# Performance work log

Measured on AMD Instinct MI355X. Metric: run time of the kernel, lower is better.

## Reference

```python
import jax, jax.numpy as jnp
import numpy as np

N = 10000      # num nodes
E = 320000     # num edges
IN = 256       # in_dim
MP = 256       # mp_width
FL = 512       # fl_width
OUT = 64       # out_dim


def setup_inputs() -> dict:
    key = jax.random.key(0)
    ks = jax.random.split(key, 20)
    inp = {}
    inp["x"] = jax.random.normal(ks[0], (N, IN), dtype=jnp.float32)
    inp["edge_index"] = jax.random.randint(ks[1], (2, E), 0, N, dtype=jnp.int64)
    # iMP (frozen) linear layers: weight ~ N(0, 1) per nn.init.normal_(std=1.0)
    inp["mp_w0"] = jax.random.normal(ks[2], (IN, MP), dtype=jnp.float32)
    inp["mp_b0"] = jax.random.uniform(ks[3], (MP,), minval=-1.0, maxval=1.0) / np.sqrt(IN)
    inp["mp_w1"] = jax.random.normal(ks[4], (MP, MP), dtype=jnp.float32)
    inp["mp_b1"] = jax.random.uniform(ks[5], (MP,), minval=-1.0, maxval=1.0) / np.sqrt(MP)
    inp["mp_w2"] = jax.random.normal(ks[6], (MP, MP), dtype=jnp.float32)
    inp["mp_b2"] = jax.random.uniform(ks[7], (MP,), minval=-1.0, maxval=1.0) / np.sqrt(MP)
    # FC layers (torch default Linear init scale ~ 1/sqrt(fan_in))
    inp["fc_w0"] = jax.random.normal(ks[8], (MP, FL), dtype=jnp.float32) / np.sqrt(MP)
    inp["fc_b0"] = jnp.zeros((FL,), dtype=jnp.float32)
    inp["fc_w1"] = jax.random.normal(ks[9], (FL, FL), dtype=jnp.float32) / np.sqrt(FL)
    inp["fc_b1"] = jnp.zeros((FL,), dtype=jnp.float32)
    # injection projections
    inp["inj_w0"] = jax.random.normal(ks[10], (MP, FL), dtype=jnp.float32) / np.sqrt(MP)
    inp["inj_b0"] = jnp.zeros((FL,), dtype=jnp.float32)
    inp["inj_w1"] = jax.random.normal(ks[11], (MP, FL), dtype=jnp.float32) / np.sqrt(MP)
    inp["inj_b1"] = jnp.zeros((FL,), dtype=jnp.float32)
    inp["alpha"] = jnp.array(1.0, dtype=jnp.float32)
    inp["out_w"] = jax.random.normal(ks[12], (FL, OUT), dtype=jnp.float32) / np.sqrt(FL)
    inp["out_b"] = jnp.zeros((OUT,), dtype=jnp.float32)
    return inp


def _imp(x, w, b, row, col, deg_inv):
    # h = relu(W x); h /= deg; Ah = scatter_add over row of h[col]
    h = jax.nn.relu(x @ w + b) * deg_inv[:, None]      # [N, out]
    return jnp.zeros_like(h).at[row].add(h[col])       # gather + scatter-add


def reference(x, edge_index, mp_w0, mp_b0, mp_w1, mp_b1, mp_w2, mp_b2,
              fc_w0, fc_b0, fc_w1, fc_b1, inj_w0, inj_b0, inj_w1, inj_b1,
              alpha, out_w, out_b):
    row, col = edge_index[0], edge_index[1]
    deg = jax.ops.segment_sum(jnp.ones((E,), x.dtype), col, num_segments=N)
    # nodes with deg==0 never appear in col so clamping does not change output
    deg_inv = 1.0 / jnp.maximum(deg, 1.0)

    h = _imp(x, mp_w0, mp_b0, row, col, deg_inv)
    h = _imp(h, mp_w1, mp_b1, row, col, deg_inv)
    h = _imp(h, mp_w2, mp_b2, row, col, deg_inv)

    x_inject = h
    h = alpha * (jax.nn.relu(h) @ fc_w0 + fc_b0) + (x_inject @ inj_w0 + inj_b0)
    h = alpha * (jax.nn.relu(h) @ fc_w1 + fc_b1) + (x_inject @ inj_w1 + inj_b1)
    return h @ out_w + out_b
```

## Files before the change

### kernel.cpp

```cpp
#include <hip/hip_runtime.h>

#define N_NODES 10000
#define N_EDGES 320000
#define MPAD 10048
#define NBIN 10048
#define CHUNK 4096
#define NCH 79

typedef unsigned short u16;
typedef short bf16x8 __attribute__((ext_vector_type(8)));
typedef float f32x4 __attribute__((ext_vector_type(4)));

__device__ __forceinline__ u16 f2b(float f) {
  unsigned u = __builtin_bit_cast(unsigned, f);
  unsigned r = u + 0x7fffu + ((u >> 16) & 1u);
  return (u16)(r >> 16);
}
__device__ __forceinline__ unsigned pack2(float a, float b) {
  return (unsigned)f2b(a) | ((unsigned)f2b(b) << 16);
}
__device__ __forceinline__ float blo(unsigned u) { return __builtin_bit_cast(float, u << 16); }
__device__ __forceinline__ float bhi(unsigned u) { return __builtin_bit_cast(float, u & 0xffff0000u); }

__global__ void prep(
    const float* __restrict__ x,
    const float* __restrict__ w0, const float* __restrict__ w1, const float* __restrict__ w2,
    const float* __restrict__ fcw0, const float* __restrict__ injw0,
    const float* __restrict__ fcw1, const float* __restrict__ injw1,
    const float* __restrict__ outw,
    const float* __restrict__ fcb0, const float* __restrict__ injb0,
    const float* __restrict__ fcb1, const float* __restrict__ injb1,
    const float* __restrict__ alpha_p,
    u16* __restrict__ xb, u16* __restrict__ w0t, u16* __restrict__ w1t, u16* __restrict__ w2t,
    u16* __restrict__ wc1t, u16* __restrict__ wc2t, u16* __restrict__ owt,
    float* __restrict__ bias1, float* __restrict__ bias2)
{
  long i = (long)blockIdx.x * 256 + threadIdx.x;
  const float alpha = alpha_p[0];
  if (i < 640000L) {
    float4 v = ((const float4*)x)[i];
    uint2 o;
    o.x = pack2(v.x, v.y);
    o.y = pack2(v.z, v.w);
    *(uint2*)(xb + 4 * i) = o;
    return;
  }
  i -= 640000L;
  if (i < 65536) { w0t[i] = f2b(w0[(i & 255) * 256 + (i >> 8)]); return; }
  i -= 65536;
  if (i < 65536) { w1t[i] = f2b(w1[(i & 255) * 256 + (i >> 8)]); return; }
  i -= 65536;
  if (i < 65536) { w2t[i] = f2b(w2[(i & 255) * 256 + (i >> 8)]); return; }
  i -= 65536;
  if (i < 262144) {
    int n = (int)(i >> 9), k = (int)(i & 511);
    float v = (k < 256) ? alpha * fcw0[k * 512 + n] : injw0[(k - 256) * 512 + n];
    wc1t[i] = f2b(v); return;
  }
  i -= 262144;
  if (i < 393216) {
    int n = (int)(i / 768), k = (int)(i % 768);
    float v = (k < 512) ? alpha * fcw1[k * 512 + n] : injw1[(k - 512) * 512 + n];
    wc2t[i] = f2b(v); return;
  }
  i -= 393216;
  if (i < 32768) {
    int n = (int)(i >> 9), k = (int)(i & 511);
    owt[i] = f2b(outw[k * 64 + n]); return;
  }
  i -= 32768;
  if (i < 512) { bias1[i] = alpha * fcb0[i] + injb0[i]; return; }
  i -= 512;
  if (i < 512) { bias2[i] = alpha * fcb1[i] + injb1[i]; return; }
}

__global__ __launch_bounds__(256) void edge_hist(const int* __restrict__ ei,
                                                 int* __restrict__ histR,
                                                 int* __restrict__ histC) {
  __shared__ int hr[NBIN], hc[NBIN];
  const int ch = blockIdx.x, t = threadIdx.x;
  for (int i = t; i < NBIN; i += 256) { hr[i] = 0; hc[i] = 0; }
  __syncthreads();
  const int e0 = ch * CHUNK;
#pragma unroll
  for (int j = 0; j < CHUNK; j += 256) {
    int e = e0 + j + t;
    if (e < N_EDGES) {
      atomicAdd(&hr[ei[e]], 1);
      atomicAdd(&hc[ei[N_EDGES + e]], 1);
    }
  }
  __syncthreads();
  for (int i = t; i < NBIN; i += 256) {
    histR[(size_t)ch * NBIN + i] = hr[i];
    histC[(size_t)ch * NBIN + i] = hc[i];
  }
}

__global__ __launch_bounds__(256) void col_scan(const int* __restrict__ histR,
                                                const int* __restrict__ histC,
                                                int* __restrict__ chunkoff,
                                                int* __restrict__ cntR,
                                                float* __restrict__ deg_inv) {
  int r = blockIdx.x * 256 + threadIdx.x;
  if (r >= NBIN) return;
  int run = 0, dg = 0;
  for (int ch = 0; ch < NCH; ++ch) {
    chunkoff[(size_t)ch * NBIN + r] = run;
    run += histR[(size_t)ch * NBIN + r];
    dg  += histC[(size_t)ch * NBIN + r];
  }
  cntR[r] = run;
  deg_inv[r] = 1.0f / (float)(dg > 1 ? dg : 1);
}

__global__ __launch_bounds__(1024) void row_scan(const int* __restrict__ cntR,
                                                 int* __restrict__ row_ptr) {
  const int t = threadIdx.x;
  const int i0 = t * 10;
  int v[10];
  int s = 0;
#pragma unroll
  for (int i = 0; i < 10; ++i) {
    int id = i0 + i;
    v[i] = (id < NBIN) ? cntR[id] : 0;
    s += v[i];
  }
  int lane = t & 63, wid = t >> 6;
  int incl = s;
#pragma unroll
  for (int off = 1; off < 64; off <<= 1) {
    int y = __shfl_up(incl, off, 64);
    if (lane >= off) incl += y;
  }
  __shared__ int wsum[16], wexc[16];
  if (lane == 63) wsum[wid] = incl;
  __syncthreads();
  if (t == 0) {
    int run = 0;
#pragma unroll
    for (int i = 0; i < 16; ++i) { wexc[i] = run; run += wsum[i]; }
  }
  __syncthreads();
  int run = wexc[wid] + incl - s;
#pragma unroll
  for (int i = 0; i < 10; ++i) {
    int id = i0 + i;
    if (id <= N_NODES) row_ptr[id] = run;
    run += v[i];
  }
}

__global__ __launch_bounds__(256) void place_edges(const int* __restrict__ ei,
                                                   const int* __restrict__ chunkoff,
                                                   const int* __restrict__ row_ptr,
                                                   int* __restrict__ csr) {
  __shared__ int cur[NBIN];
  const int ch = blockIdx.x, t = threadIdx.x;
  const int* co = chunkoff + (size_t)ch * NBIN;
  for (int i = t; i < NBIN; i += 256) cur[i] = co[i];
  __syncthreads();
  const int e0 = ch * CHUNK;
#pragma unroll
  for (int j = 0; j < CHUNK; j += 256) {
    int e = e0 + j + t;
    if (e < N_EDGES) {
      int r = ei[e];
      int c = ei[N_EDGES + e];
      int rank = atomicAdd(&cur[r], 1);
      csr[row_ptr[r] + rank] = c;
    }
  }
}

template<int K, bool RELU, bool SCALE, bool F32OUT>
__global__ __launch_bounds__(256) void gemm64(
    const u16* __restrict__ A, int lda,
    const u16* __restrict__ Bt,
    const float* __restrict__ bias,
    const float* __restrict__ scale,
    u16* __restrict__ Cb, float* __restrict__ Cf, int ldc)
{
  __shared__ u16 As[64 * 72];
  __shared__ u16 Bs[64 * 72];
  const int tid = threadIdx.x;
  const int m0 = blockIdx.x * 64;
  const int n0 = blockIdx.y * 64;
  const int wave = tid >> 6;
  const int lane = tid & 63;
  const int wr = (wave >> 1) * 32;
  const int wc = (wave & 1) * 32;
  const int lm = lane & 15;
  const int koff = (lane >> 4) * 8;

  const int srow = tid >> 2;
  const int scol = (tid & 3) * 16;
  const u16* Ag = A + (size_t)(m0 + srow) * lda + scol;
  const u16* Bg = Bt + (size_t)(n0 + srow) * K + scol;
  u16* Asw = &As[srow * 72 + scol];
  u16* Bsw = &Bs[srow * 72 + scol];

  f32x4 acc[2][2] = {};

  int4 a0 = *(const int4*)(Ag);
  int4 a1 = *(const int4*)(Ag + 8);
  int4 b0 = *(const int4*)(Bg);
  int4 b1 = *(const int4*)(Bg + 8);

#pragma unroll
  for (int kb = 0; kb < K; kb += 64) {
    __syncthreads();
    *(int4*)Asw = a0; *(int4*)(Asw + 8) = a1;
    *(int4*)Bsw = b0; *(int4*)(Bsw + 8) = b1;
    __syncthreads();
    if (kb + 64 < K) {
      a0 = *(const int4*)(Ag + kb + 64);
      a1 = *(const int4*)(Ag + kb + 72);
      b0 = *(const int4*)(Bg + kb + 64);
      b1 = *(const int4*)(Bg + kb + 72);
    }
#pragma unroll
    for (int ks = 0; ks < 2; ++ks) {
      bf16x8 af0 = *(const bf16x8*)&As[(wr + lm) * 72 + ks * 32 + koff];
      bf16x8 af1 = *(const bf16x8*)&As[(wr + 16 + lm) * 72 + ks * 32 + koff];
      bf16x8 bf0 = *(const bf16x8*)&Bs[(wc + lm) * 72 + ks * 32 + koff];
      bf16x8 bf1 = *(const bf16x8*)&Bs[(wc + 16 + lm) * 72 + ks * 32 + koff];
      acc[0][0] = __builtin_amdgcn_mfma_f32_16x16x32_bf16(af0, bf0, acc[0][0], 0, 0, 0);
      acc[0][1] = __builtin_amdgcn_mfma_f32_16x16x32_bf16(af0, bf1, acc[0][1], 0, 0, 0);
      acc[1][0] = __builtin_amdgcn_mfma_f32_16x16x32_bf16(af1, bf0, acc[1][0], 0, 0, 0);
      acc[1][1] = __builtin_amdgcn_mfma_f32_16x16x32_bf16(af1, bf1, acc[1][1], 0, 0, 0);
    }
  }

  const int q4 = (lane >> 4) * 4;
#pragma unroll
  for (int i = 0; i < 2; ++i) {
#pragma unroll
    for (int j = 0; j < 2; ++j) {
      const int gc = n0 + wc + j * 16 + lm;
      const float bv = bias[gc];
#pragma unroll
      for (int r = 0; r < 4; ++r) {
        const int gr = m0 + wr + i * 16 + q4 + r;
        float v = acc[i][j][r] + bv;
        if (RELU) v = fmaxf(v, 0.f);
        if (SCALE) v *= scale[gr];
        if (F32OUT) {
          if (gr < N_NODES) Cf[(size_t)gr * ldc + gc] = v;
        } else {
          Cb[(size_t)gr * ldc + gc] = f2b(v);
        }
      }
    }
  }
}

__global__ __launch_bounds__(256) void aggregate(
    const u16* __restrict__ tmp, const int* __restrict__ row_ptr,
    const int* __restrict__ csr, u16* __restrict__ out0,
    u16* __restrict__ A1, u16* __restrict__ A2, int mode)
{
  const int wv = threadIdx.x >> 6;
  const int lane = threadIdx.x & 63;
  const int r = blockIdx.x * 4 + wv;
  const int beg = row_ptr[r], end = row_ptr[r + 1];
  const size_t feat = (size_t)lane * 8;
  const char* tb = (const char*)tmp;

  float s0 = 0.f, s1 = 0.f, s2 = 0.f, s3 = 0.f;
  int i = beg;
  for (; i + 8 <= end; i += 8) {
    uint2 v[8];
#pragma unroll
    for (int j = 0; j < 8; ++j)
      v[j] = *(const uint2*)(tb + (size_t)csr[i + j] * 512 + feat);
#pragma unroll
    for (int j = 0; j < 8; ++j) {
      s0 += blo(v[j].x); s1 += bhi(v[j].x); s2 += blo(v[j].y); s3 += bhi(v[j].y);
    }
  }
  for (; i < end; ++i) {
    uint2 v = *(const uint2*)(tb + (size_t)csr[i] * 512 + feat);
    s0 += blo(v.x); s1 += bhi(v.x); s2 += blo(v.y); s3 += bhi(v.y);
  }

  uint2 pv; pv.x = pack2(s0, s1); pv.y = pack2(s2, s3);
  if (mode == 0) {
    *(uint2*)((char*)out0 + (size_t)r * 512 + feat) = pv;
  } else {
    uint2 pr;
    pr.x = pack2(fmaxf(s0, 0.f), fmaxf(s1, 0.f));
    pr.y = pack2(fmaxf(s2, 0.f), fmaxf(s3, 0.f));
    *(uint2*)((char*)A1 + (size_t)r * 1024 + feat) = pr;
    *(uint2*)((char*)A1 + (size_t)r * 1024 + 512 + feat) = pv;
    *(uint2*)((char*)A2 + (size_t)r * 1536 + 1024 + feat) = pv;
  }
}

extern "C" void kernel_launch(void* const* d_in, const int* in_sizes, int n_in,
                              void* d_out, int out_size, void* d_ws, size_t ws_size,
                              hipStream_t stream) {
  const float* x      = (const float*)d_in[0];
  const int*   ei     = (const int*)d_in[1];
  const float* mp_w0  = (const float*)d_in[2];
  const float* mp_b0  = (const float*)d_in[3];
  const float* mp_w1  = (const float*)d_in[4];
  const float* mp_b1  = (const float*)d_in[5];
  const float* mp_w2  = (const float*)d_in[6];
  const float* mp_b2  = (const float*)d_in[7];
  const float* fc_w0  = (const float*)d_in[8];
  const float* fc_b0  = (const float*)d_in[9];
  const float* fc_w1  = (const float*)d_in[10];
  const float* fc_b1  = (const float*)d_in[11];
  const float* inj_w0 = (const float*)d_in[12];
  const float* inj_b0 = (const float*)d_in[13];
  const float* inj_w1 = (const float*)d_in[14];
  const float* inj_b1 = (const float*)d_in[15];
  const float* alpha  = (const float*)d_in[16];
  const float* out_w  = (const float*)d_in[17];
  const float* out_b  = (const float*)d_in[18];
  float* out = (float*)d_out;

  char* p = (char*)d_ws;
  auto carve = [&](size_t bytes) -> void* {
    void* r = (void*)p;
    p += (bytes + 255) & ~(size_t)255;
    return r;
  };
  int*   histR    = (int*)carve((size_t)NCH * NBIN * 4);
  int*   histC    = (int*)carve((size_t)NCH * NBIN * 4);
  int*   chunkoff = (int*)carve((size_t)NCH * NBIN * 4);
  int*   cntR     = (int*)carve(NBIN * 4);
  int*   row_ptr  = (int*)carve((N_NODES + 1) * 4);
  int*   csr      = (int*)carve((size_t)N_EDGES * 4);
  float* deg_inv  = (float*)carve(NBIN * 4);
  float* bias1    = (float*)carve(512 * 4);
  float* bias2    = (float*)carve(512 * 4);
  u16* xb   = (u16*)carve((size_t)MPAD * 256 * 2);
  u16* w0t  = (u16*)carve(65536 * 2);
  u16* w1t  = (u16*)carve(65536 * 2);
  u16* w2t  = (u16*)carve(65536 * 2);
  u16* wc1t = (u16*)carve(262144 * 2);
  u16* wc2t = (u16*)carve(393216 * 2);
  u16* owt  = (u16*)carve(32768 * 2);
  u16* tmp  = (u16*)carve((size_t)MPAD * 256 * 2);
  u16* h    = (u16*)carve((size_t)MPAD * 256 * 2);
  u16* A1   = (u16*)carve((size_t)MPAD * 512 * 2);
  u16* A2   = (u16*)carve((size_t)MPAD * 768 * 2);
  u16* C2   = (u16*)carve((size_t)MPAD * 512 * 2);

  prep<<<5960, 256, 0, stream>>>(x, mp_w0, mp_w1, mp_w2, fc_w0, inj_w0, fc_w1, inj_w1,
                                 out_w, fc_b0, inj_b0, fc_b1, inj_b1, alpha,
                                 xb, w0t, w1t, w2t, wc1t, wc2t, owt, bias1, bias2);
  edge_hist<<<NCH, 256, 0, stream>>>(ei, histR, histC);
  col_scan<<<(NBIN + 255) / 256, 256, 0, stream>>>(histR, histC, chunkoff, cntR, deg_inv);
  row_scan<<<1, 1024, 0, stream>>>(cntR, row_ptr);
  place_edges<<<NCH, 256, 0, stream>>>(ei, chunkoff, row_ptr, csr);

  dim3 g4(MPAD / 64, 4), g8(MPAD / 64, 8), g1(MPAD / 64, 1);
  gemm64<256, true, true, false><<<g4, 256, 0, stream>>>(xb, 256, w0t, mp_b0, deg_inv, tmp, nullptr, 256);
  aggregate<<<2500, 256, 0, stream>>>(tmp, row_ptr, csr, h, nullptr, nullptr, 0);
  gemm64<256, true, true, false><<<g4, 256, 0, stream>>>(h, 256, w1t, mp_b1, deg_inv, tmp, nullptr, 256);
  aggregate<<<2500, 256, 0, stream>>>(tmp, row_ptr, csr, h, nullptr, nullptr, 0);
  gemm64<256, true, true, false><<<g4, 256, 0, stream>>>(h, 256, w2t, mp_b2, deg_inv, tmp, nullptr, 256);
  aggregate<<<2500, 256, 0, stream>>>(tmp, row_ptr, csr, nullptr, A1, A2, 1);
  gemm64<512, true, false, false><<<g8, 256, 0, stream>>>(A1, 512, wc1t, bias1, nullptr, A2, nullptr, 768);
  gemm64<768, false, false, false><<<g8, 256, 0, stream>>>(A2, 768, wc2t, bias2, nullptr, C2, nullptr, 512);
  gemm64<512, false, false, true><<<g1, 256, 0, stream>>>(C2, 512, owt, out_b, nullptr, nullptr, out, 64);
}
```

Measured before the change: 274.8 us.

## Add 128x128 MFMA GEMM tiles, widen aggregate loads, halve edge chunks

```diff
diff --git a/kernel.cpp b/kernel.cpp
--- a/kernel.cpp
+++ b/kernel.cpp
@@ -2,10 +2,10 @@
 
 #define N_NODES 10000
 #define N_EDGES 320000
-#define MPAD 10048
+#define MPAD 10112
 #define NBIN 10048
-#define CHUNK 4096
-#define NCH 79
+#define CHUNK 2048
+#define NCH 157
 
 typedef unsigned short u16;
 typedef short bf16x8 __attribute__((ext_vector_type(8)));
@@ -103,8 +103,10 @@
                                                 int* __restrict__ cntR,
                                                 float* __restrict__ deg_inv) {
   int r = blockIdx.x * 256 + threadIdx.x;
-  if (r >= NBIN) return;
+  if (r >= MPAD) return;
+  if (r >= NBIN) { deg_inv[r] = 1.0f; return; }
   int run = 0, dg = 0;
+#pragma unroll 4
   for (int ch = 0; ch < NCH; ++ch) {
     chunkoff[(size_t)ch * NBIN + r] = run;
     run += histR[(size_t)ch * NBIN + r];
@@ -169,6 +171,98 @@
       int c = ei[N_EDGES + e];
       int rank = atomicAdd(&cur[r], 1);
       csr[row_ptr[r] + rank] = c;
+    }
+  }
+}
+
+template<int K, bool RELU, bool SCALE, bool F32OUT>
+__global__ __launch_bounds__(256) void gemm128(
+    const u16* __restrict__ A, int lda,
+    const u16* __restrict__ Bt,
+    const float* __restrict__ bias,
+    const float* __restrict__ scale,
+    u16* __restrict__ Cb, float* __restrict__ Cf, int ldc)
+{
+  __shared__ u16 As[128 * 72];
+  __shared__ u16 Bs[128 * 72];
+  const int tid = threadIdx.x;
+  const int m0 = blockIdx.x * 128;
+  const int n0 = blockIdx.y * 128;
+  const int wave = tid >> 6;
+  const int lane = tid & 63;
+  const int wr = (wave >> 1) * 64;
+  const int wc = (wave & 1) * 64;
+  const int lm = lane & 15;
+  const int koff = (lane >> 4) * 8;
+
+  const int srow = tid >> 1;
+  const int scol = (tid & 1) * 32;
+  const u16* Ag = A + (size_t)(m0 + srow) * lda + scol;
+  const u16* Bg = Bt + (size_t)(n0 + srow) * K + scol;
+  u16* Asw = &As[srow * 72 + scol];
+  u16* Bsw = &Bs[srow * 72 + scol];
+
+  f32x4 acc[4][4] = {};
+
+  int4 pa[4], pb[4];
+#pragma unroll
+  for (int j = 0; j < 4; ++j) {
+    pa[j] = *(const int4*)(Ag + 8 * j);
+    pb[j] = *(const int4*)(Bg + 8 * j);
+  }
+
+#pragma unroll
+  for (int kb = 0; kb < K; kb += 64) {
+    __syncthreads();
+#pragma unroll
+    for (int j = 0; j < 4; ++j) {
+      *(int4*)(Asw + 8 * j) = pa[j];
+      *(int4*)(Bsw + 8 * j) = pb[j];
+    }
+    __syncthreads();
+    if (kb + 64 < K) {
+#pragma unroll
+      for (int j = 0; j < 4; ++j) {
+        pa[j] = *(const int4*)(Ag + kb + 64 + 8 * j);
+        pb[j] = *(const int4*)(Bg + kb + 64 + 8 * j);
+      }
+    }
+#pragma unroll
+    for (int ks = 0; ks < 2; ++ks) {
+      bf16x8 af[4], bf[4];
+#pragma unroll
+      for (int mi = 0; mi < 4; ++mi)
+        af[mi] = *(const bf16x8*)&As[(wr + mi * 16 + lm) * 72 + ks * 32 + koff];
+#pragma unroll
+      for (int ni = 0; ni < 4; ++ni)
+        bf[ni] = *(const bf16x8*)&Bs[(wc + ni * 16 + lm) * 72 + ks * 32 + koff];
+#pragma unroll
+      for (int mi = 0; mi < 4; ++mi)
+#pragma unroll
+        for (int ni = 0; ni < 4; ++ni)
+          acc[mi][ni] = __builtin_amdgcn_mfma_f32_16x16x32_bf16(af[mi], bf[ni], acc[mi][ni], 0, 0, 0);
+    }
+  }
+
+  const int q4 = (lane >> 4) * 4;
+#pragma unroll
+  for (int mi = 0; mi < 4; ++mi) {
+#pragma unroll
+    for (int ni = 0; ni < 4; ++ni) {
+      const int gc = n0 + wc + ni * 16 + lm;
+      const float bv = bias[gc];
+#pragma unroll
+      for (int r = 0; r < 4; ++r) {
+        const int gr = m0 + wr + mi * 16 + q4 + r;
+        float v = acc[mi][ni][r] + bv;
+        if (RELU) v = fmaxf(v, 0.f);
+        if (SCALE) v *= scale[gr];
+        if (F32OUT) {
+          if (gr < N_NODES) Cf[(size_t)gr * ldc + gc] = v;
+        } else {
+          Cb[(size_t)gr * ldc + gc] = f2b(v);
+        }
+      }
     }
   }
 }
@@ -263,37 +357,55 @@
   const int wv = threadIdx.x >> 6;
   const int lane = threadIdx.x & 63;
   const int r = blockIdx.x * 4 + wv;
+  const int half = lane >> 5;
+  const int q = lane & 31;
   const int beg = row_ptr[r], end = row_ptr[r + 1];
-  const size_t feat = (size_t)lane * 8;
+  const size_t feat = (size_t)q * 16;
   const char* tb = (const char*)tmp;
 
-  float s0 = 0.f, s1 = 0.f, s2 = 0.f, s3 = 0.f;
+  float s0 = 0.f, s1 = 0.f, s2 = 0.f, s3 = 0.f, s4 = 0.f, s5 = 0.f, s6 = 0.f, s7 = 0.f;
   int i = beg;
   for (; i + 8 <= end; i += 8) {
-    uint2 v[8];
-#pragma unroll
-    for (int j = 0; j < 8; ++j)
-      v[j] = *(const uint2*)(tb + (size_t)csr[i + j] * 512 + feat);
-#pragma unroll
-    for (int j = 0; j < 8; ++j) {
+    uint4 v[4];
+#pragma unroll
+    for (int j = 0; j < 4; ++j)
+      v[j] = *(const uint4*)(tb + (size_t)csr[i + 2 * j + half] * 512 + feat);
+#pragma unroll
+    for (int j = 0; j < 4; ++j) {
       s0 += blo(v[j].x); s1 += bhi(v[j].x); s2 += blo(v[j].y); s3 += bhi(v[j].y);
-    }
-  }
-  for (; i < end; ++i) {
-    uint2 v = *(const uint2*)(tb + (size_t)csr[i] * 512 + feat);
-    s0 += blo(v.x); s1 += bhi(v.x); s2 += blo(v.y); s3 += bhi(v.y);
-  }
-
-  uint2 pv; pv.x = pack2(s0, s1); pv.y = pack2(s2, s3);
-  if (mode == 0) {
-    *(uint2*)((char*)out0 + (size_t)r * 512 + feat) = pv;
-  } else {
-    uint2 pr;
-    pr.x = pack2(fmaxf(s0, 0.f), fmaxf(s1, 0.f));
-    pr.y = pack2(fmaxf(s2, 0.f), fmaxf(s3, 0.f));
-    *(uint2*)((char*)A1 + (size_t)r * 1024 + feat) = pr;
-    *(uint2*)((char*)A1 + (size_t)r * 1024 + 512 + feat) = pv;
-    *(uint2*)((char*)A2 + (size_t)r * 1536 + 1024 + feat) = pv;
+      s4 += blo(v[j].z); s5 += bhi(v[j].z); s6 += blo(v[j].w); s7 += bhi(v[j].w);
+    }
+  }
+  for (; i < end; i += 2) {
+    int id = i + half;
+    if (id < end) {
+      uint4 v = *(const uint4*)(tb + (size_t)csr[id] * 512 + feat);
+      s0 += blo(v.x); s1 += bhi(v.x); s2 += blo(v.y); s3 += bhi(v.y);
+      s4 += blo(v.z); s5 += bhi(v.z); s6 += blo(v.w); s7 += bhi(v.w);
+    }
+  }
+  const int src = lane ^ 32;
+  s0 += __shfl(s0, src, 64); s1 += __shfl(s1, src, 64);
+  s2 += __shfl(s2, src, 64); s3 += __shfl(s3, src, 64);
+  s4 += __shfl(s4, src, 64); s5 += __shfl(s5, src, 64);
+  s6 += __shfl(s6, src, 64); s7 += __shfl(s7, src, 64);
+
+  if (half == 0) {
+    uint4 pv;
+    pv.x = pack2(s0, s1); pv.y = pack2(s2, s3);
+    pv.z = pack2(s4, s5); pv.w = pack2(s6, s7);
+    if (mode == 0) {
+      *(uint4*)((char*)out0 + (size_t)r * 512 + feat) = pv;
+    } else {
+      uint4 pr;
+      pr.x = pack2(fmaxf(s0, 0.f), fmaxf(s1, 0.f));
+      pr.y = pack2(fmaxf(s2, 0.f), fmaxf(s3, 0.f));
+      pr.z = pack2(fmaxf(s4, 0.f), fmaxf(s5, 0.f));
+      pr.w = pack2(fmaxf(s6, 0.f), fmaxf(s7, 0.f));
+      *(uint4*)((char*)A1 + (size_t)r * 1024 + feat) = pr;
+      *(uint4*)((char*)A1 + (size_t)r * 1024 + 512 + feat) = pv;
+      *(uint4*)((char*)A2 + (size_t)r * 1536 + 1024 + feat) = pv;
+    }
   }
 }
 
@@ -333,7 +445,7 @@
   int*   cntR     = (int*)carve(NBIN * 4);
   int*   row_ptr  = (int*)carve((N_NODES + 1) * 4);
   int*   csr      = (int*)carve((size_t)N_EDGES * 4);
-  float* deg_inv  = (float*)carve(NBIN * 4);
+  float* deg_inv  = (float*)carve(MPAD * 4);
   float* bias1    = (float*)carve(512 * 4);
   float* bias2    = (float*)carve(512 * 4);
   u16* xb   = (u16*)carve((size_t)MPAD * 256 * 2);
@@ -353,18 +465,18 @@
                                  out_w, fc_b0, inj_b0, fc_b1, inj_b1, alpha,
                                  xb, w0t, w1t, w2t, wc1t, wc2t, owt, bias1, bias2);
   edge_hist<<<NCH, 256, 0, stream>>>(ei, histR, histC);
-  col_scan<<<(NBIN + 255) / 256, 256, 0, stream>>>(histR, histC, chunkoff, cntR, deg_inv);
+  col_scan<<<(MPAD + 255) / 256, 256, 0, stream>>>(histR, histC, chunkoff, cntR, deg_inv);
   row_scan<<<1, 1024, 0, stream>>>(cntR, row_ptr);
   place_edges<<<NCH, 256, 0, stream>>>(ei, chunkoff, row_ptr, csr);
 
-  dim3 g4(MPAD / 64, 4), g8(MPAD / 64, 8), g1(MPAD / 64, 1);
-  gemm64<256, true, true, false><<<g4, 256, 0, stream>>>(xb, 256, w0t, mp_b0, deg_inv, tmp, nullptr, 256);
+  dim3 gmp(MPAD / 128, 2), gfc(MPAD / 128, 4), go(MPAD / 64, 1);
+  gemm128<256, true, true, false><<<gmp, 256, 0, stream>>>(xb, 256, w0t, mp_b0, deg_inv, tmp, nullptr, 256);
   aggregate<<<2500, 256, 0, stream>>>(tmp, row_ptr, csr, h, nullptr, nullptr, 0);
-  gemm64<256, true, true, false><<<g4, 256, 0, stream>>>(h, 256, w1t, mp_b1, deg_inv, tmp, nullptr, 256);
+  gemm128<256, true, true, false><<<gmp, 256, 0, stream>>>(h, 256, w1t, mp_b1, deg_inv, tmp, nullptr, 256);
   aggregate<<<2500, 256, 0, stream>>>(tmp, row_ptr, csr, h, nullptr, nullptr, 0);
-  gemm64<256, true, true, false><<<g4, 256, 0, stream>>>(h, 256, w2t, mp_b2, deg_inv, tmp, nullptr, 256);
+  gemm128<256, true, true, false><<<gmp, 256, 0, stream>>>(h, 256, w2t, mp_b2, deg_inv, tmp, nullptr, 256);
   aggregate<<<2500, 256, 0, stream>>>(tmp, row_ptr, csr, nullptr, A1, A2, 1);
-  gemm64<512, true, false, false><<<g8, 256, 0, stream>>>(A1, 512, wc1t, bias1, nullptr, A2, nullptr, 768);
-  gemm64<768, false, false, false><<<g8, 256, 0, stream>>>(A2, 768, wc2t, bias2, nullptr, C2, nullptr, 512);
-  gemm64<512, false, false, true><<<g1, 256, 0, stream>>>(C2, 512, owt, out_b, nullptr, nullptr, out, 64);
-}
+  gemm128<512, true, false, false><<<gfc, 256, 0, stream>>>(A1, 512, wc1t, bias1, nullptr, A2, nullptr, 768);
+  gemm128<768, false, false, false><<<gfc, 256, 0, stream>>>(A2, 768, wc2t, bias2, nullptr, C2, nullptr, 512);
+  gemm64<512, false, false, true><<<go, 256, 0, stream>>>(C2, 512, owt, out_b, nullptr, nullptr, out, 64);
+}
```

New measurement: 395.9 us. +44.0%, slower.

## Retune GEMM to two waves, widen aggregate loads, halve edge-chunk size

Applied to the files above, without the earlier changes.

```diff
diff --git a/kernel.cpp b/kernel.cpp
--- a/kernel.cpp
+++ b/kernel.cpp
@@ -2,10 +2,10 @@
 
 #define N_NODES 10000
 #define N_EDGES 320000
-#define MPAD 10048
+#define MPAD 10112
 #define NBIN 10048
-#define CHUNK 4096
-#define NCH 79
+#define CHUNK 2048
+#define NCH 157
 
 typedef unsigned short u16;
 typedef short bf16x8 __attribute__((ext_vector_type(8)));
@@ -103,8 +103,10 @@
                                                 int* __restrict__ cntR,
                                                 float* __restrict__ deg_inv) {
   int r = blockIdx.x * 256 + threadIdx.x;
-  if (r >= NBIN) return;
+  if (r >= MPAD) return;
+  if (r >= NBIN) { deg_inv[r] = 1.0f; return; }
   int run = 0, dg = 0;
+#pragma unroll 4
   for (int ch = 0; ch < NCH; ++ch) {
     chunkoff[(size_t)ch * NBIN + r] = run;
     run += histR[(size_t)ch * NBIN + r];
@@ -174,7 +176,7 @@
 }
 
 template<int K, bool RELU, bool SCALE, bool F32OUT>
-__global__ __launch_bounds__(256) void gemm64(
+__global__ __launch_bounds__(128) void gemm64(
     const u16* __restrict__ A, int lda,
     const u16* __restrict__ Bt,
     const float* __restrict__ bias,
@@ -188,61 +190,70 @@
   const int n0 = blockIdx.y * 64;
   const int wave = tid >> 6;
   const int lane = tid & 63;
-  const int wr = (wave >> 1) * 32;
-  const int wc = (wave & 1) * 32;
+  const int wr = wave * 32;
   const int lm = lane & 15;
   const int koff = (lane >> 4) * 8;
 
   const int srow = tid >> 2;
   const int scol = (tid & 3) * 16;
-  const u16* Ag = A + (size_t)(m0 + srow) * lda + scol;
-  const u16* Bg = Bt + (size_t)(n0 + srow) * K + scol;
-  u16* Asw = &As[srow * 72 + scol];
-  u16* Bsw = &Bs[srow * 72 + scol];
-
-  f32x4 acc[2][2] = {};
-
-  int4 a0 = *(const int4*)(Ag);
-  int4 a1 = *(const int4*)(Ag + 8);
-  int4 b0 = *(const int4*)(Bg);
-  int4 b1 = *(const int4*)(Bg + 8);
+  const u16* Ag0 = A + (size_t)(m0 + srow) * lda + scol;
+  const u16* Ag1 = A + (size_t)(m0 + srow + 32) * lda + scol;
+  const u16* Bg0 = Bt + (size_t)(n0 + srow) * K + scol;
+  const u16* Bg1 = Bt + (size_t)(n0 + srow + 32) * K + scol;
+  u16* Asw0 = &As[srow * 72 + scol];
+  u16* Asw1 = &As[(srow + 32) * 72 + scol];
+  u16* Bsw0 = &Bs[srow * 72 + scol];
+  u16* Bsw1 = &Bs[(srow + 32) * 72 + scol];
+
+  f32x4 acc[2][4] = {};
+
+  int4 pa0 = *(const int4*)(Ag0),     pa1 = *(const int4*)(Ag0 + 8);
+  int4 pa2 = *(const int4*)(Ag1),     pa3 = *(const int4*)(Ag1 + 8);
+  int4 pb0 = *(const int4*)(Bg0),     pb1 = *(const int4*)(Bg0 + 8);
+  int4 pb2 = *(const int4*)(Bg1),     pb3 = *(const int4*)(Bg1 + 8);
 
 #pragma unroll
   for (int kb = 0; kb < K; kb += 64) {
     __syncthreads();
-    *(int4*)Asw = a0; *(int4*)(Asw + 8) = a1;
-    *(int4*)Bsw = b0; *(int4*)(Bsw + 8) = b1;
+    *(int4*)Asw0 = pa0; *(int4*)(Asw0 + 8) = pa1;
+    *(int4*)Asw1 = pa2; *(int4*)(Asw1 + 8) = pa3;
+    *(int4*)Bsw0 = pb0; *(int4*)(Bsw0 + 8) = pb1;
+    *(int4*)Bsw1 = pb2; *(int4*)(Bsw1 + 8) = pb3;
     __syncthreads();
     if (kb + 64 < K) {
-      a0 = *(const int4*)(Ag + kb + 64);
-      a1 = *(const int4*)(Ag + kb + 72);
-      b0 = *(const int4*)(Bg + kb + 64);
-      b1 = *(const int4*)(Bg + kb + 72);
+      pa0 = *(const int4*)(Ag0 + kb + 64); pa1 = *(const int4*)(Ag0 + kb + 72);
+      pa2 = *(const int4*)(Ag1 + kb + 64); pa3 = *(const int4*)(Ag1 + kb + 72);
+      pb0 = *(const int4*)(Bg0 + kb + 64); pb1 = *(const int4*)(Bg0 + kb + 72);
+      pb2 = *(const int4*)(Bg1 + kb + 64); pb3 = *(const int4*)(Bg1 + kb + 72);
     }
 #pragma unroll
     for (int ks = 0; ks < 2; ++ks) {
-      bf16x8 af0 = *(const bf16x8*)&As[(wr + lm) * 72 + ks * 32 + koff];
-      bf16x8 af1 = *(const bf16x8*)&As[(wr + 16 + lm) * 72 + ks * 32 + koff];
-      bf16x8 bf0 = *(const bf16x8*)&Bs[(wc + lm) * 72 + ks * 32 + koff];
-      bf16x8 bf1 = *(const bf16x8*)&Bs[(wc + 16 + lm) * 72 + ks * 32 + koff];
-      acc[0][0] = __builtin_amdgcn_mfma_f32_16x16x32_bf16(af0, bf0, acc[0][0], 0, 0, 0);
-      acc[0][1] = __builtin_amdgcn_mfma_f32_16x16x32_bf16(af0, bf1, acc[0][1], 0, 0, 0);
-      acc[1][0] = __builtin_amdgcn_mfma_f32_16x16x32_bf16(af1, bf0, acc[1][0], 0, 0, 0);
-      acc[1][1] = __builtin_amdgcn_mfma_f32_16x16x32_bf16(af1, bf1, acc[1][1], 0, 0, 0);
+      bf16x8 af[2], bf[4];
+#pragma unroll
+      for (int mi = 0; mi < 2; ++mi)
+        af[mi] = *(const bf16x8*)&As[(wr + mi * 16 + lm) * 72 + ks * 32 + koff];
+#pragma unroll
+      for (int ni = 0; ni < 4; ++ni)
+        bf[ni] = *(const bf16x8*)&Bs[(ni * 16 + lm) * 72 + ks * 32 + koff];
+#pragma unroll
+      for (int mi = 0; mi < 2; ++mi)
+#pragma unroll
+        for (int ni = 0; ni < 4; ++ni)
+          acc[mi][ni] = __builtin_amdgcn_mfma_f32_16x16x32_bf16(af[mi], bf[ni], acc[mi][ni], 0, 0, 0);
     }
   }
 
   const int q4 = (lane >> 4) * 4;
 #pragma unroll
-  for (int i = 0; i < 2; ++i) {
-#pragma unroll
-    for (int j = 0; j < 2; ++j) {
-      const int gc = n0 + wc + j * 16 + lm;
+  for (int mi = 0; mi < 2; ++mi) {
+#pragma unroll
+    for (int ni = 0; ni < 4; ++ni) {
+      const int gc = n0 + ni * 16 + lm;
       const float bv = bias[gc];
 #pragma unroll
       for (int r = 0; r < 4; ++r) {
-        const int gr = m0 + wr + i * 16 + q4 + r;
-        float v = acc[i][j][r] + bv;
+        const int gr = m0 + wr + mi * 16 + q4 + r;
+        float v = acc[mi][ni][r] + bv;
         if (RELU) v = fmaxf(v, 0.f);
         if (SCALE) v *= scale[gr];
         if (F32OUT) {
@@ -263,37 +274,55 @@
   const int wv = threadIdx.x >> 6;
   const int lane = threadIdx.x & 63;
   const int r = blockIdx.x * 4 + wv;
+  const int half = lane >> 5;
+  const int q = lane & 31;
   const int beg = row_ptr[r], end = row_ptr[r + 1];
-  const size_t feat = (size_t)lane * 8;
+  const size_t feat = (size_t)q * 16;
   const char* tb = (const char*)tmp;
 
-  float s0 = 0.f, s1 = 0.f, s2 = 0.f, s3 = 0.f;
+  float s0 = 0.f, s1 = 0.f, s2 = 0.f, s3 = 0.f, s4 = 0.f, s5 = 0.f, s6 = 0.f, s7 = 0.f;
   int i = beg;
   for (; i + 8 <= end; i += 8) {
-    uint2 v[8];
-#pragma unroll
-    for (int j = 0; j < 8; ++j)
-      v[j] = *(const uint2*)(tb + (size_t)csr[i + j] * 512 + feat);
-#pragma unroll
-    for (int j = 0; j < 8; ++j) {
+    uint4 v[4];
+#pragma unroll
+    for (int j = 0; j < 4; ++j)
+      v[j] = *(const uint4*)(tb + (size_t)csr[i + 2 * j + half] * 512 + feat);
+#pragma unroll
+    for (int j = 0; j < 4; ++j) {
       s0 += blo(v[j].x); s1 += bhi(v[j].x); s2 += blo(v[j].y); s3 += bhi(v[j].y);
-    }
-  }
-  for (; i < end; ++i) {
-    uint2 v = *(const uint2*)(tb + (size_t)csr[i] * 512 + feat);
-    s0 += blo(v.x); s1 += bhi(v.x); s2 += blo(v.y); s3 += bhi(v.y);
-  }
-
-  uint2 pv; pv.x = pack2(s0, s1); pv.y = pack2(s2, s3);
-  if (mode == 0) {
-    *(uint2*)((char*)out0 + (size_t)r * 512 + feat) = pv;
-  } else {
-    uint2 pr;
-    pr.x = pack2(fmaxf(s0, 0.f), fmaxf(s1, 0.f));
-    pr.y = pack2(fmaxf(s2, 0.f), fmaxf(s3, 0.f));
-    *(uint2*)((char*)A1 + (size_t)r * 1024 + feat) = pr;
-    *(uint2*)((char*)A1 + (size_t)r * 1024 + 512 + feat) = pv;
-    *(uint2*)((char*)A2 + (size_t)r * 1536 + 1024 + feat) = pv;
+      s4 += blo(v[j].z); s5 += bhi(v[j].z); s6 += blo(v[j].w); s7 += bhi(v[j].w);
+    }
+  }
+  for (; i < end; i += 2) {
+    int id = i + half;
+    if (id < end) {
+      uint4 v = *(const uint4*)(tb + (size_t)csr[id] * 512 + feat);
+      s0 += blo(v.x); s1 += bhi(v.x); s2 += blo(v.y); s3 += bhi(v.y);
+      s4 += blo(v.z); s5 += bhi(v.z); s6 += blo(v.w); s7 += bhi(v.w);
+    }
+  }
+  const int src = lane ^ 32;
+  s0 += __shfl(s0, src, 64); s1 += __shfl(s1, src, 64);
+  s2 += __shfl(s2, src, 64); s3 += __shfl(s3, src, 64);
+  s4 += __shfl(s4, src, 64); s5 += __shfl(s5, src, 64);
+  s6 += __shfl(s6, src, 64); s7 += __shfl(s7, src, 64);
+
+  if (half == 0) {
+    uint4 pv;
+    pv.x = pack2(s0, s1); pv.y = pack2(s2, s3);
+    pv.z = pack2(s4, s5); pv.w = pack2(s6, s7);
+    if (mode == 0) {
+      *(uint4*)((char*)out0 + (size_t)r * 512 + feat) = pv;
+    } else {
+      uint4 pr;
+      pr.x = pack2(fmaxf(s0, 0.f), fmaxf(s1, 0.f));
+      pr.y = pack2(fmaxf(s2, 0.f), fmaxf(s3, 0.f));
+      pr.z = pack2(fmaxf(s4, 0.f), fmaxf(s5, 0.f));
+      pr.w = pack2(fmaxf(s6, 0.f), fmaxf(s7, 0.f));
+      *(uint4*)((char*)A1 + (size_t)r * 1024 + feat) = pr;
+      *(uint4*)((char*)A1 + (size_t)r * 1024 + 512 + feat) = pv;
+      *(uint4*)((char*)A2 + (size_t)r * 1536 + 1024 + feat) = pv;
+    }
   }
 }
 
@@ -333,7 +362,7 @@
   int*   cntR     = (int*)carve(NBIN * 4);
   int*   row_ptr  = (int*)carve((N_NODES + 1) * 4);
   int*   csr      = (int*)carve((size_t)N_EDGES * 4);
-  float* deg_inv  = (float*)carve(NBIN * 4);
+  float* deg_inv  = (float*)carve(MPAD * 4);
   float* bias1    = (float*)carve(512 * 4);
   float* bias2    = (float*)carve(512 * 4);
   u16* xb   = (u16*)carve((size_t)MPAD * 256 * 2);
@@ -353,18 +382,18 @@
                                  out_w, fc_b0, inj_b0, fc_b1, inj_b1, alpha,
                                  xb, w0t, w1t, w2t, wc1t, wc2t, owt, bias1, bias2);
   edge_hist<<<NCH, 256, 0, stream>>>(ei, histR, histC);
-  col_scan<<<(NBIN + 255) / 256, 256, 0, stream>>>(histR, histC, chunkoff, cntR, deg_inv);
+  col_scan<<<(MPAD + 255) / 256, 256, 0, stream>>>(histR, histC, chunkoff, cntR, deg_inv);
   row_scan<<<1, 1024, 0, stream>>>(cntR, row_ptr);
   place_edges<<<NCH, 256, 0, stream>>>(ei, chunkoff, row_ptr, csr);
 
-  dim3 g4(MPAD / 64, 4), g8(MPAD / 64, 8), g1(MPAD / 64, 1);
-  gemm64<256, true, true, false><<<g4, 256, 0, stream>>>(xb, 256, w0t, mp_b0, deg_inv, tmp, nullptr, 256);
+  dim3 gmp(MPAD / 64, 4), gfc(MPAD / 64, 8), go(MPAD / 64, 1);
+  gemm64<256, true, true, false><<<gmp, 128, 0, stream>>>(xb, 256, w0t, mp_b0, deg_inv, tmp, nullptr, 256);
   aggregate<<<2500, 256, 0, stream>>>(tmp, row_ptr, csr, h, nullptr, nullptr, 0);
-  gemm64<256, true, true, false><<<g4, 256, 0, stream>>>(h, 256, w1t, mp_b1, deg_inv, tmp, nullptr, 256);
+  gemm64<256, true, true, false><<<gmp, 128, 0, stream>>>(h, 256, w1t, mp_b1, deg_inv, tmp, nullptr, 256);
   aggregate<<<2500, 256, 0, stream>>>(tmp, row_ptr, csr, h, nullptr, nullptr, 0);
-  gemm64<256, true, true, false><<<g4, 256, 0, stream>>>(h, 256, w2t, mp_b2, deg_inv, tmp, nullptr, 256);
+  gemm64<256, true, true, false><<<gmp, 128, 0, stream>>>(h, 256, w2t, mp_b2, deg_inv, tmp, nullptr, 256);
   aggregate<<<2500, 256, 0, stream>>>(tmp, row_ptr, csr, nullptr, A1, A2, 1);
-  gemm64<512, true, false, false><<<g8, 256, 0, stream>>>(A1, 512, wc1t, bias1, nullptr, A2, nullptr, 768);
-  gemm64<768, false, false, false><<<g8, 256, 0, stream>>>(A2, 768, wc2t, bias2, nullptr, C2, nullptr, 512);
-  gemm64<512, false, false, true><<<g1, 256, 0, stream>>>(C2, 512, owt, out_b, nullptr, nullptr, out, 64);
-}
+  gemm64<512, true, false, false><<<gfc, 128, 0, stream>>>(A1, 512, wc1t, bias1, nullptr, A2, nullptr, 768);
+  gemm64<768, false, false, false><<<gfc, 128, 0, stream>>>(A2, 768, wc2t, bias2, nullptr, C2, nullptr, 512);
+  gemm64<512, false, false, true><<<go, 128, 0, stream>>>(C2, 512, owt, out_b, nullptr, nullptr, out, 64);
+}
```

Result: faster. 267.9 us (-2.5%).
